# Optimization experiments

Hardware: AMD Instinct MI355X
Metric: run time of the kernel (lower is better)

The kernel has to match this reference:

```python
import jax, jax.numpy as jnp
import numpy as np

B, S, D, CH = 2048, 16, 512, 1024


def setup_inputs() -> dict:
    key = jax.random.key(0)
    ks = jax.random.split(key, 12)
    sc = lambda fan: 1.0 / np.sqrt(fan)
    return {
        "local_descs_t": jax.random.normal(ks[0], (B, S, D), jnp.float32),
        "local_descs_rot": jax.random.normal(ks[1], (B, S, D), jnp.float32),
        "w_scene": jax.random.normal(ks[2], (2 * D,), jnp.float32) * sc(2 * D),
        "b_scene": jnp.zeros((1,), jnp.float32),
        "Wh_t": jax.random.normal(ks[3], (S, D, CH), jnp.float32) * sc(D),
        "bh_t": jnp.zeros((S, CH), jnp.float32),
        "Wo_t": jax.random.normal(ks[4], (S, CH, 3), jnp.float32) * sc(CH),
        "bo_t": jnp.zeros((S, 3), jnp.float32),
        "Wh_r": jax.random.normal(ks[5], (S, D, CH), jnp.float32) * sc(D),
        "bh_r": jnp.zeros((S, CH), jnp.float32),
        "Wo_r": jax.random.normal(ks[6], (S, CH, 4), jnp.float32) * sc(CH),
        "bo_r": jnp.zeros((S, 4), jnp.float32),
    }


def _expert_head(x, onehot, Wh, bh, Wo, bo):
    # x: [B, D] gathered global descriptor; run all S experts, combine by one-hot
    h = jax.nn.gelu(jnp.einsum("bd,sdh->bsh", x, Wh) + bh, approximate=False)
    o = jnp.einsum("bsh,sho->bso", h, Wo) + bo  # [B, S, out]
    return jnp.einsum("bs,bso->bo", onehot, o)


def reference(local_descs_t, local_descs_rot, w_scene, b_scene,
              Wh_t, bh_t, Wo_t, bo_t, Wh_r, bh_r, Wo_r, bo_r):
    # scene router: Linear(2D -> 1) over concatenated descriptors, log_softmax over scenes
    cat = jnp.concatenate([local_descs_t, local_descs_rot], axis=2)  # [B, S, 2D]
    logits = jnp.einsum("bsd,d->bs", cat, w_scene) + b_scene[0]
    scene_log_distr = jax.nn.log_softmax(logits, axis=1)  # [B, S]
    max_indices = jnp.argmax(scene_log_distr, axis=1)  # [B]
    onehot = jax.nn.one_hot(max_indices, S, dtype=local_descs_t.dtype)
    # combine: gather selected scene's descriptor (torch code uses dense mask w)
    global_desc_t = jnp.einsum("bs,bsd->bd", onehot, local_descs_t)
    global_desc_rot = jnp.einsum("bs,bsd->bd", onehot, local_descs_rot)
    # per-sample expert heads (Linear -> GELU -> Linear)
    x_t = _expert_head(global_desc_t, onehot, Wh_t, bh_t, Wo_t, bo_t)    # [B, 3]
    x_rot = _expert_head(global_desc_rot, onehot, Wh_r, bh_r, Wo_r, bo_r)  # [B, 4]
    pose = jnp.concatenate([x_t, x_rot], axis=1)  # [B, 7]
    return pose, scene_log_distr
```

## Files before the change

### kernel.cpp

```cpp
#include <hip/hip_runtime.h>
#include <hip/hip_bf16.h>
#include <math.h>

constexpr int B_  = 2048;
constexpr int S_  = 16;
constexpr int D_  = 512;
constexpr int CH_ = 1024;

typedef __attribute__((ext_vector_type(8))) short bf16x8;
typedef __attribute__((ext_vector_type(4))) float f32x4;

constexpr size_t CNT_OFF  = 0;
constexpr size_t NT_OFF   = 64;
constexpr size_t TL_OFF   = 128;
constexpr size_t LIST_OFF = 512;
constexpr size_t XGT_OFF  = LIST_OFF + (size_t)16 * 2048 * 4;
constexpr size_t XGR_OFF  = XGT_OFF + (size_t)B_ * D_ * 2;

static __device__ __forceinline__ short f2bf(float x) {
    __hip_bfloat16 h = __float2bfloat16(x);
    return *(short*)&h;
}
static __device__ __forceinline__ float gelu_exact(float x) {
    return 0.5f * x * (1.f + erff(x * 0.70710678118654752f));
}

static __device__ __forceinline__ void gl_lds16(const void* g, void* l) {
    __builtin_amdgcn_global_load_lds(
        (const __attribute__((address_space(1))) void*)g,
        (__attribute__((address_space(3))) void*)l,
        16, 0, 0);
}

__global__ __launch_bounds__(1024) void k_router_sm(
    const float* __restrict__ ldt, const float* __restrict__ ldr,
    const float* __restrict__ w,   const float* __restrict__ bsc,
    float* __restrict__ sld, int* __restrict__ count, int* __restrict__ list,
    unsigned short* __restrict__ xgt, unsigned short* __restrict__ xgr,
    float* __restrict__ pose)
{
    const int b    = blockIdx.x;
    const int wave = threadIdx.x >> 6;
    const int lane = threadIdx.x & 63;

    __shared__ float lgs[S_];
    __shared__ int   smi;

    if (threadIdx.x < 7) pose[(size_t)b * 7 + threadIdx.x] = 0.f;

    const float4* pt = (const float4*)(ldt + ((size_t)b * S_ + wave) * D_);
    const float4* pr = (const float4*)(ldr + ((size_t)b * S_ + wave) * D_);
    const float4* wt = (const float4*)(w);
    const float4* wr = (const float4*)(w + D_);

    float acc = 0.f;
    #pragma unroll
    for (int it = 0; it < 2; it++) {
        const int i = lane + it * 64;
        float4 a  = pt[i]; float4 ww = wt[i];
        acc += a.x * ww.x + a.y * ww.y + a.z * ww.z + a.w * ww.w;
        float4 c  = pr[i]; float4 w2 = wr[i];
        acc += c.x * w2.x + c.y * w2.y + c.z * w2.z + c.w * w2.w;
    }
    #pragma unroll
    for (int off = 32; off > 0; off >>= 1) acc += __shfl_down(acc, off, 64);
    if (lane == 0) lgs[wave] = acc;
    __syncthreads();

    if (threadIdx.x < S_) {
        const int s = threadIdx.x;
        const float v = lgs[s] + bsc[0];
        float mv = v; int mi = s;
        #pragma unroll
        for (int d = 1; d < 16; d <<= 1) {
            float ov = __shfl_xor(mv, d, 16);
            int   oi = __shfl_xor(mi, d, 16);
            if (ov > mv || (ov == mv && oi < mi)) { mv = ov; mi = oi; }
        }
        float sum = expf(v - mv);
        #pragma unroll
        for (int d = 1; d < 16; d <<= 1) sum += __shfl_xor(sum, d, 16);
        const float lse = mv + logf(sum);
        sld[b * S_ + s] = v - lse;
        if (s == 0) {
            smi = mi;
            const int pos = atomicAdd(&count[mi], 1);
            list[mi * B_ + pos] = b;
        }
    }
    __syncthreads();

    const int mi = smi;
    const int t = threadIdx.x;
    if (t < D_) {
        xgt[(size_t)b * D_ + t] = (unsigned short)f2bf(ldt[((size_t)b * S_ + mi) * D_ + t]);
    } else {
        const int t2 = t - D_;
        xgr[(size_t)b * D_ + t2] = (unsigned short)f2bf(ldr[((size_t)b * S_ + mi) * D_ + t2]);
    }
}

__global__ void k_tiles(const int* __restrict__ count, int* __restrict__ ntile,
                        int* __restrict__ tlist)
{
    if (threadIdx.x == 0 && blockIdx.x == 0) {
        int nt = 0;
        for (int m = 0; m < S_; m++) {
            const int c = count[m];
            const int nst = (c + 63) >> 6;
            for (int s2 = 0; s2 < nst; s2++) tlist[nt++] = m | (s2 << 8);
        }
        ntile[0] = nt;
    }
}

__global__ __launch_bounds__(256) void k_expert(
    const float* __restrict__ Wht, const float* __restrict__ bht,
    const float* __restrict__ Wot, const float* __restrict__ bot,
    const float* __restrict__ Whr, const float* __restrict__ bhr,
    const float* __restrict__ Wor, const float* __restrict__ bor,
    const unsigned short* __restrict__ xgt, const unsigned short* __restrict__ xgr,
    const int* __restrict__ count, const int* __restrict__ list,
    const int* __restrict__ ntile, const int* __restrict__ tlist,
    float* __restrict__ pose)
{
    const int bid  = blockIdx.x;
    const int ct   = bid & 15;
    const int head = (bid >> 4) & 1;
    const int t    = bid >> 5;
    if (t >= ntile[0]) return;
    const int tv = tlist[t];
    const int m  = tv & 255;
    const int st = tv >> 8;
    const int n  = count[m];

    const unsigned short* __restrict__ xg = head ? xgr : xgt;
    const float* __restrict__ Wh = head ? Whr : Wht;
    const float* __restrict__ bh = head ? bhr : bht;
    const float* __restrict__ Wo = head ? Wor : Wot;
    const float* __restrict__ bo = head ? bor : bot;
    const int noj    = head ? 4 : 3;
    const int jobase = head ? 3 : 0;
    const int ch0    = ct * 64;

    __shared__ short As[64 * 64];
    __shared__ float Bsf[64 * 64];
    __shared__ float ored[64][4];
    __shared__ int   bidx[64];

    const int tid  = threadIdx.x;
    const int wave = tid >> 6;
    const int lane = tid & 63;
    const int l15  = lane & 15;
    const int lq   = lane >> 4;
    const int wr   = wave >> 1, wc = wave & 1;
    const int rbase = wr * 32, cbase = wc * 32;

    if (tid < 64) {
        const int gi = st * 64 + tid;
        bidx[tid] = (gi < n) ? list[m * B_ + gi] : list[m * B_];
    }
    ((float*)ored)[tid] = 0.f;
    __syncthreads();

    const unsigned short* gA[2];
    #pragma unroll
    for (int i = 0; i < 2; i++) {
        const int r = (wave * 2 + i) * 8 + (lane >> 3);
        const int c = (lane & 7) ^ (r & 7);
        gA[i] = xg + (size_t)bidx[r] * D_ + c * 8;
    }
    const float* gB[4];
    #pragma unroll
    for (int i = 0; i < 4; i++) {
        const int q2 = wave * 4 + i;
        gB[i] = Wh + (size_t)m * D_ * CH_ + (size_t)(q2 * 4 + (lane >> 4)) * CH_ + ch0 + (l15 * 4);
    }

    f32x4 acc[2][2] = {};

    for (int kt = 0; kt < 8; kt++) {
        const int k0 = kt * 64;
        #pragma unroll
        for (int i = 0; i < 2; i++)
            gl_lds16(gA[i] + k0, &As[(wave * 2 + i) * 512]);
        #pragma unroll
        for (int i = 0; i < 4; i++)
            gl_lds16(gB[i] + (size_t)k0 * CH_, &Bsf[(wave * 4 + i) * 256]);
        __syncthreads();

        #pragma unroll
        for (int ks = 0; ks < 2; ks++) {
            bf16x8 a[2];
            #pragma unroll
            for (int fm = 0; fm < 2; fm++) {
                const int r = rbase + fm * 16 + l15;
                const int u = ks * 4 + lq;
                a[fm] = *(const bf16x8*)&As[r * 64 + ((u ^ (r & 7)) << 3)];
            }
            bf16x8 bv[2];
            #pragma unroll
            for (int fn = 0; fn < 2; fn++) {
                const int c = cbase + fn * 16 + l15;
                const int kb = ks * 32 + lq * 8;
                short tmp[8];
                #pragma unroll
                for (int j = 0; j < 8; j++) tmp[j] = f2bf(Bsf[(kb + j) * 64 + c]);
                bv[fn] = *(bf16x8*)tmp;
            }
            #pragma unroll
            for (int fm = 0; fm < 2; fm++)
                #pragma unroll
                for (int fn = 0; fn < 2; fn++)
                    acc[fm][fn] = __builtin_amdgcn_mfma_f32_16x16x32_bf16(a[fm], bv[fn], acc[fm][fn], 0, 0, 0);
        }
        __syncthreads();
    }

    float g[2][2][4];
    float wo_l[2][4];
    #pragma unroll
    for (int fn = 0; fn < 2; fn++) {
        const int ch = ch0 + cbase + fn * 16 + l15;
        const float bias = bh[m * CH_ + ch];
        #pragma unroll
        for (int fm = 0; fm < 2; fm++)
            #pragma unroll
            for (int j = 0; j < 4; j++)
                g[fm][fn][j] = gelu_exact(acc[fm][fn][j] + bias);
        #pragma unroll
        for (int jo = 0; jo < 4; jo++)
            wo_l[fn][jo] = (jo < noj) ? Wo[(size_t)(m * CH_ + ch) * noj + jo] : 0.f;
    }

    #pragma unroll
    for (int fm = 0; fm < 2; fm++) {
        #pragma unroll
        for (int j = 0; j < 4; j++) {
            const int rl = rbase + fm * 16 + lq * 4 + j;
            #pragma unroll
            for (int jo = 0; jo < 4; jo++) {
                if (jo >= noj) continue;
                float v = g[fm][0][j] * wo_l[0][jo] + g[fm][1][j] * wo_l[1][jo];
                #pragma unroll
                for (int d = 1; d < 16; d <<= 1) v += __shfl_xor(v, d, 16);
                if (l15 == 0)
                    atomicAdd(&ored[rl][jo], v);
            }
        }
    }
    __syncthreads();

    {
        const int rl = tid >> 2;
        const int jo = tid & 3;
        const int gi = st * 64 + rl;
        if (jo < noj && gi < n) {
            const int bb = list[m * B_ + gi];
            float v = ored[rl][jo];
            if (ct == 0) v += bo[m * noj + jo];
            atomicAdd(&pose[(size_t)bb * 7 + jobase + jo], v);
        }
    }
}

extern "C" void kernel_launch(void* const* d_in, const int* in_sizes, int n_in,
                              void* d_out, int out_size, void* d_ws, size_t ws_size,
                              hipStream_t stream)
{
    const float* ldt = (const float*)d_in[0];
    const float* ldr = (const float*)d_in[1];
    const float* wsc = (const float*)d_in[2];
    const float* bsc = (const float*)d_in[3];
    const float* Wht = (const float*)d_in[4];
    const float* bht = (const float*)d_in[5];
    const float* Wot = (const float*)d_in[6];
    const float* bot = (const float*)d_in[7];
    const float* Whr = (const float*)d_in[8];
    const float* bhr = (const float*)d_in[9];
    const float* Wor = (const float*)d_in[10];
    const float* bor = (const float*)d_in[11];

    float* pose = (float*)d_out;
    float* sld  = (float*)d_out + (size_t)B_ * 7;

    int* count = (int*)((char*)d_ws + CNT_OFF);
    int* ntile = (int*)((char*)d_ws + NT_OFF);
    int* tlist = (int*)((char*)d_ws + TL_OFF);
    int* list  = (int*)((char*)d_ws + LIST_OFF);
    unsigned short* xgt = (unsigned short*)((char*)d_ws + XGT_OFF);
    unsigned short* xgr = (unsigned short*)((char*)d_ws + XGR_OFF);

    (void)hipMemsetAsync(count, 0, 16 * sizeof(int), stream);

    k_router_sm<<<dim3(B_), dim3(1024), 0, stream>>>(
        ldt, ldr, wsc, bsc, sld, count, list, xgt, xgr, pose);

    k_tiles<<<dim3(1), dim3(64), 0, stream>>>(count, ntile, tlist);

    k_expert<<<dim3(48 * 2 * 16), dim3(256), 0, stream>>>(
        Wht, bht, Wot, bot, Whr, bhr, Wor, bor,
        xgt, xgr, count, list, ntile, tlist, pose);
}
```

Before: 78.12 us.

## Fuse tile-list build into router via last-block counter and shrink router blocks

The separate single-thread k_tiles kernel is removed. The router kernel's last-finishing block, found through a global done counter with a threadfence and atomic, now builds the tile list, which saves one kernel launch and its dependency gap. The router block size drops from 1024 to 256 threads, so each wave reduces four scenes, and the descriptor gather and bf16 conversion now use float4 loads with short4 stores. The memset is widened to also clear the done counter. This relies on correct atomic visibility of count across blocks.

Result: slower. 133.3 us (+70.6%).

```diff
diff --git a/kernel.cpp b/kernel.cpp
--- a/kernel.cpp
+++ b/kernel.cpp
@@ -11,7 +11,8 @@
 typedef __attribute__((ext_vector_type(4))) float f32x4;
 
 constexpr size_t CNT_OFF  = 0;
-constexpr size_t NT_OFF   = 64;
+constexpr size_t DONE_OFF = 64;
+constexpr size_t NT_OFF   = 96;
 constexpr size_t TL_OFF   = 128;
 constexpr size_t LIST_OFF = 512;
 constexpr size_t XGT_OFF  = LIST_OFF + (size_t)16 * 2048 * 4;
@@ -32,43 +33,55 @@
         16, 0, 0);
 }
 
-__global__ __launch_bounds__(1024) void k_router_sm(
+__global__ __launch_bounds__(256) void k_router_sm(
     const float* __restrict__ ldt, const float* __restrict__ ldr,
     const float* __restrict__ w,   const float* __restrict__ bsc,
     float* __restrict__ sld, int* __restrict__ count, int* __restrict__ list,
     unsigned short* __restrict__ xgt, unsigned short* __restrict__ xgr,
-    float* __restrict__ pose)
+    float* __restrict__ pose, int* __restrict__ done,
+    int* __restrict__ ntile, int* __restrict__ tlist)
 {
     const int b    = blockIdx.x;
-    const int wave = threadIdx.x >> 6;
-    const int lane = threadIdx.x & 63;
+    const int tid  = threadIdx.x;
+    const int wave = tid >> 6;
+    const int lane = tid & 63;
 
     __shared__ float lgs[S_];
     __shared__ int   smi;
 
-    if (threadIdx.x < 7) pose[(size_t)b * 7 + threadIdx.x] = 0.f;
-
-    const float4* pt = (const float4*)(ldt + ((size_t)b * S_ + wave) * D_);
-    const float4* pr = (const float4*)(ldr + ((size_t)b * S_ + wave) * D_);
+    if (tid < 7) pose[(size_t)b * 7 + tid] = 0.f;
+
     const float4* wt = (const float4*)(w);
     const float4* wr = (const float4*)(w + D_);
 
-    float acc = 0.f;
-    #pragma unroll
-    for (int it = 0; it < 2; it++) {
-        const int i = lane + it * 64;
-        float4 a  = pt[i]; float4 ww = wt[i];
-        acc += a.x * ww.x + a.y * ww.y + a.z * ww.z + a.w * ww.w;
-        float4 c  = pr[i]; float4 w2 = wr[i];
-        acc += c.x * w2.x + c.y * w2.y + c.z * w2.z + c.w * w2.w;
-    }
-    #pragma unroll
-    for (int off = 32; off > 0; off >>= 1) acc += __shfl_down(acc, off, 64);
-    if (lane == 0) lgs[wave] = acc;
-    __syncthreads();
-
-    if (threadIdx.x < S_) {
-        const int s = threadIdx.x;
+    float accv[4];
+    #pragma unroll
+    for (int it = 0; it < 4; it++) {
+        const int s = wave * 4 + it;
+        const float4* pt = (const float4*)(ldt + ((size_t)b * S_ + s) * D_);
+        const float4* pr = (const float4*)(ldr + ((size_t)b * S_ + s) * D_);
+        float a = 0.f;
+        #pragma unroll
+        for (int half = 0; half < 2; half++) {
+            const int i = lane + half * 64;
+            const float4 x  = pt[i]; const float4 ww = wt[i];
+            a += x.x * ww.x + x.y * ww.y + x.z * ww.z + x.w * ww.w;
+            const float4 y  = pr[i]; const float4 w2 = wr[i];
+            a += y.x * w2.x + y.y * w2.y + y.z * w2.z + y.w * w2.w;
+        }
+        accv[it] = a;
+    }
+    #pragma unroll
+    for (int it = 0; it < 4; it++) {
+        float a = accv[it];
+        #pragma unroll
+        for (int off = 32; off > 0; off >>= 1) a += __shfl_down(a, off, 64);
+        if (lane == 0) lgs[wave * 4 + it] = a;
+    }
+    __syncthreads();
+
+    if (tid < S_) {
+        const int s = tid;
         const float v = lgs[s] + bsc[0];
         float mv = v; int mi = s;
         #pragma unroll
@@ -91,26 +104,29 @@
     __syncthreads();
 
     const int mi = smi;
-    const int t = threadIdx.x;
-    if (t < D_) {
-        xgt[(size_t)b * D_ + t] = (unsigned short)f2bf(ldt[((size_t)b * S_ + mi) * D_ + t]);
+    if (tid < 128) {
+        const float4 v = ((const float4*)(ldt + ((size_t)b * S_ + mi) * D_))[tid];
+        short4 o; o.x = f2bf(v.x); o.y = f2bf(v.y); o.z = f2bf(v.z); o.w = f2bf(v.w);
+        *reinterpret_cast<short4*>(&xgt[(size_t)b * D_ + (size_t)tid * 4]) = o;
     } else {
-        const int t2 = t - D_;
-        xgr[(size_t)b * D_ + t2] = (unsigned short)f2bf(ldr[((size_t)b * S_ + mi) * D_ + t2]);
-    }
-}
-
-__global__ void k_tiles(const int* __restrict__ count, int* __restrict__ ntile,
-                        int* __restrict__ tlist)
-{
-    if (threadIdx.x == 0 && blockIdx.x == 0) {
-        int nt = 0;
-        for (int m = 0; m < S_; m++) {
-            const int c = count[m];
-            const int nst = (c + 63) >> 6;
-            for (int s2 = 0; s2 < nst; s2++) tlist[nt++] = m | (s2 << 8);
-        }
-        ntile[0] = nt;
+        const int t2 = tid - 128;
+        const float4 v = ((const float4*)(ldr + ((size_t)b * S_ + mi) * D_))[t2];
+        short4 o; o.x = f2bf(v.x); o.y = f2bf(v.y); o.z = f2bf(v.z); o.w = f2bf(v.w);
+        *reinterpret_cast<short4*>(&xgr[(size_t)b * D_ + (size_t)t2 * 4]) = o;
+    }
+    __syncthreads();
+
+    if (tid == 0) {
+        __threadfence();
+        if (atomicAdd(done, 1) == (int)gridDim.x - 1) {
+            int nt = 0;
+            for (int mm = 0; mm < S_; mm++) {
+                const int c = atomicAdd(&count[mm], 0);
+                const int nst = (c + 63) >> 6;
+                for (int s2 = 0; s2 < nst; s2++) tlist[nt++] = mm | (s2 << 8);
+            }
+            ntile[0] = nt;
+        }
     }
 }
 
@@ -285,18 +301,17 @@
     float* sld  = (float*)d_out + (size_t)B_ * 7;
 
     int* count = (int*)((char*)d_ws + CNT_OFF);
+    int* done  = (int*)((char*)d_ws + DONE_OFF);
     int* ntile = (int*)((char*)d_ws + NT_OFF);
     int* tlist = (int*)((char*)d_ws + TL_OFF);
     int* list  = (int*)((char*)d_ws + LIST_OFF);
     unsigned short* xgt = (unsigned short*)((char*)d_ws + XGT_OFF);
     unsigned short* xgr = (unsigned short*)((char*)d_ws + XGR_OFF);
 
-    (void)hipMemsetAsync(count, 0, 16 * sizeof(int), stream);
-
-    k_router_sm<<<dim3(B_), dim3(1024), 0, stream>>>(
-        ldt, ldr, wsc, bsc, sld, count, list, xgt, xgr, pose);
-
-    k_tiles<<<dim3(1), dim3(64), 0, stream>>>(count, ntile, tlist);
+    (void)hipMemsetAsync(d_ws, 0, 128, stream);
+
+    k_router_sm<<<dim3(B_), dim3(256), 0, stream>>>(
+        ldt, ldr, wsc, bsc, sld, count, list, xgt, xgr, pose, done, ntile, tlist);
 
     k_expert<<<dim3(48 * 2 * 16), dim3(256), 0, stream>>>(
         Wht, bht, Wot, bot, Whr, bhr, Wor, bor,
```

## Split router into batched logits kernel and per-sample finish kernel

Applied to the files above, without the earlier changes.

The fused 1024-thread router kernel is replaced by two kernels. k_logits has each wave handle four (batch, scene) rows, with the scene weights hoisted into registers and all row loads issued before any reduction, to raise memory-level parallelism on the large descriptor stream. k_finish uses one wave per sample to do log-softmax, argmax, list append and a vectorized bf16 gather of the selected rows. The cost is an extra kernel launch, a small logits round trip through workspace, and a second read of the selected descriptor rows.

Measured after the change: 90.73 us. 1.16x slower.

```diff
diff --git a/kernel.cpp b/kernel.cpp
--- a/kernel.cpp
+++ b/kernel.cpp
@@ -11,9 +11,10 @@
 typedef __attribute__((ext_vector_type(4))) float f32x4;
 
 constexpr size_t CNT_OFF  = 0;
-constexpr size_t NT_OFF   = 64;
+constexpr size_t NT_OFF   = 96;
 constexpr size_t TL_OFF   = 128;
-constexpr size_t LIST_OFF = 512;
+constexpr size_t LOG_OFF  = 384;
+constexpr size_t LIST_OFF = LOG_OFF + (size_t)B_ * S_ * 4;
 constexpr size_t XGT_OFF  = LIST_OFF + (size_t)16 * 2048 * 4;
 constexpr size_t XGR_OFF  = XGT_OFF + (size_t)B_ * D_ * 2;
 
@@ -23,6 +24,9 @@
 }
 static __device__ __forceinline__ float gelu_exact(float x) {
     return 0.5f * x * (1.f + erff(x * 0.70710678118654752f));
+}
+static __device__ __forceinline__ float dot4(float4 a, float4 b) {
+    return a.x * b.x + a.y * b.y + a.z * b.z + a.w * b.w;
 }
 
 static __device__ __forceinline__ void gl_lds16(const void* g, void* l) {
@@ -32,71 +36,83 @@
         16, 0, 0);
 }
 
-__global__ __launch_bounds__(1024) void k_router_sm(
+__global__ __launch_bounds__(256, 4) void k_logits(
     const float* __restrict__ ldt, const float* __restrict__ ldr,
     const float* __restrict__ w,   const float* __restrict__ bsc,
+    float* __restrict__ logits)
+{
+    const int lane = threadIdx.x & 63;
+    const int wid  = blockIdx.x * 4 + (threadIdx.x >> 6);
+    const int p0   = wid * 4;
+
+    const float4* wt = (const float4*)w;
+    const float4 wv0 = wt[lane];
+    const float4 wv1 = wt[lane + 64];
+    const float4 wv2 = wt[lane + 128];
+    const float4 wv3 = wt[lane + 192];
+    const float bias = bsc[0];
+
+    float4 xt[4][2], xr[4][2];
+    #pragma unroll
+    for (int k = 0; k < 4; k++) {
+        const float4* pt = (const float4*)(ldt + (size_t)(p0 + k) * D_);
+        const float4* pr = (const float4*)(ldr + (size_t)(p0 + k) * D_);
+        xt[k][0] = pt[lane]; xt[k][1] = pt[lane + 64];
+        xr[k][0] = pr[lane]; xr[k][1] = pr[lane + 64];
+    }
+    #pragma unroll
+    for (int k = 0; k < 4; k++) {
+        float a = dot4(xt[k][0], wv0) + dot4(xt[k][1], wv1)
+                + dot4(xr[k][0], wv2) + dot4(xr[k][1], wv3);
+        #pragma unroll
+        for (int off = 32; off > 0; off >>= 1) a += __shfl_down(a, off, 64);
+        if (lane == 0) logits[p0 + k] = a + bias;
+    }
+}
+
+__global__ __launch_bounds__(256) void k_finish(
+    const float* __restrict__ ldt, const float* __restrict__ ldr,
+    const float* __restrict__ logits,
     float* __restrict__ sld, int* __restrict__ count, int* __restrict__ list,
     unsigned short* __restrict__ xgt, unsigned short* __restrict__ xgr,
     float* __restrict__ pose)
 {
-    const int b    = blockIdx.x;
     const int wave = threadIdx.x >> 6;
     const int lane = threadIdx.x & 63;
-
-    __shared__ float lgs[S_];
-    __shared__ int   smi;
-
-    if (threadIdx.x < 7) pose[(size_t)b * 7 + threadIdx.x] = 0.f;
-
-    const float4* pt = (const float4*)(ldt + ((size_t)b * S_ + wave) * D_);
-    const float4* pr = (const float4*)(ldr + ((size_t)b * S_ + wave) * D_);
-    const float4* wt = (const float4*)(w);
-    const float4* wr = (const float4*)(w + D_);
-
-    float acc = 0.f;
-    #pragma unroll
-    for (int it = 0; it < 2; it++) {
-        const int i = lane + it * 64;
-        float4 a  = pt[i]; float4 ww = wt[i];
-        acc += a.x * ww.x + a.y * ww.y + a.z * ww.z + a.w * ww.w;
-        float4 c  = pr[i]; float4 w2 = wr[i];
-        acc += c.x * w2.x + c.y * w2.y + c.z * w2.z + c.w * w2.w;
-    }
-    #pragma unroll
-    for (int off = 32; off > 0; off >>= 1) acc += __shfl_down(acc, off, 64);
-    if (lane == 0) lgs[wave] = acc;
-    __syncthreads();
-
-    if (threadIdx.x < S_) {
-        const int s = threadIdx.x;
-        const float v = lgs[s] + bsc[0];
-        float mv = v; int mi = s;
-        #pragma unroll
-        for (int d = 1; d < 16; d <<= 1) {
-            float ov = __shfl_xor(mv, d, 16);
-            int   oi = __shfl_xor(mi, d, 16);
-            if (ov > mv || (ov == mv && oi < mi)) { mv = ov; mi = oi; }
-        }
-        float sum = expf(v - mv);
-        #pragma unroll
-        for (int d = 1; d < 16; d <<= 1) sum += __shfl_xor(sum, d, 16);
-        const float lse = mv + logf(sum);
-        sld[b * S_ + s] = v - lse;
-        if (s == 0) {
-            smi = mi;
-            const int pos = atomicAdd(&count[mi], 1);
-            list[mi * B_ + pos] = b;
-        }
-    }
-    __syncthreads();
-
-    const int mi = smi;
-    const int t = threadIdx.x;
-    if (t < D_) {
-        xgt[(size_t)b * D_ + t] = (unsigned short)f2bf(ldt[((size_t)b * S_ + mi) * D_ + t]);
-    } else {
-        const int t2 = t - D_;
-        xgr[(size_t)b * D_ + t2] = (unsigned short)f2bf(ldr[((size_t)b * S_ + mi) * D_ + t2]);
+    const int b    = blockIdx.x * 4 + wave;
+
+    float v = (lane < S_) ? logits[b * S_ + lane] : -INFINITY;
+    float mv = v; int mi_ = lane;
+    #pragma unroll
+    for (int d = 1; d < 16; d <<= 1) {
+        float ov = __shfl_xor(mv, d, 16);
+        int   oi = __shfl_xor(mi_, d, 16);
+        if (ov > mv || (ov == mv && oi < mi_)) { mv = ov; mi_ = oi; }
+    }
+    float e = (lane < S_) ? expf(v - mv) : 0.f;
+    float sum = e;
+    #pragma unroll
+    for (int d = 1; d < 16; d <<= 1) sum += __shfl_xor(sum, d, 16);
+    if (lane < S_) sld[b * S_ + lane] = v - (mv + logf(sum));
+
+    const int mi = __shfl(mi_, 0, 64);
+    if (lane == 0) {
+        const int pos = atomicAdd(&count[mi], 1);
+        list[mi * B_ + pos] = b;
+    }
+    if (lane < 7) pose[(size_t)b * 7 + lane] = 0.f;
+
+    const float4* pt = (const float4*)(ldt + ((size_t)b * S_ + mi) * D_);
+    const float4* pr = (const float4*)(ldr + ((size_t)b * S_ + mi) * D_);
+    #pragma unroll
+    for (int h = 0; h < 2; h++) {
+        const int i = lane + h * 64;
+        const float4 a = pt[i];
+        short4 o1; o1.x = f2bf(a.x); o1.y = f2bf(a.y); o1.z = f2bf(a.z); o1.w = f2bf(a.w);
+        *reinterpret_cast<short4*>(&xgt[(size_t)b * D_ + (size_t)i * 4]) = o1;
+        const float4 c = pr[i];
+        short4 o2; o2.x = f2bf(c.x); o2.y = f2bf(c.y); o2.z = f2bf(c.z); o2.w = f2bf(c.w);
+        *reinterpret_cast<short4*>(&xgr[(size_t)b * D_ + (size_t)i * 4]) = o2;
     }
 }
 
@@ -284,17 +300,20 @@
     float* pose = (float*)d_out;
     float* sld  = (float*)d_out + (size_t)B_ * 7;
 
-    int* count = (int*)((char*)d_ws + CNT_OFF);
-    int* ntile = (int*)((char*)d_ws + NT_OFF);
-    int* tlist = (int*)((char*)d_ws + TL_OFF);
-    int* list  = (int*)((char*)d_ws + LIST_OFF);
+    int*   count  = (int*)((char*)d_ws + CNT_OFF);
+    int*   ntile  = (int*)((char*)d_ws + NT_OFF);
+    int*   tlist  = (int*)((char*)d_ws + TL_OFF);
+    float* logits = (float*)((char*)d_ws + LOG_OFF);
+    int*   list   = (int*)((char*)d_ws + LIST_OFF);
     unsigned short* xgt = (unsigned short*)((char*)d_ws + XGT_OFF);
     unsigned short* xgr = (unsigned short*)((char*)d_ws + XGR_OFF);
 
-    (void)hipMemsetAsync(count, 0, 16 * sizeof(int), stream);
-
-    k_router_sm<<<dim3(B_), dim3(1024), 0, stream>>>(
-        ldt, ldr, wsc, bsc, sld, count, list, xgt, xgr, pose);
+    (void)hipMemsetAsync(count, 0, 64, stream);
+
+    k_logits<<<dim3(B_ * S_ / 16), dim3(256), 0, stream>>>(ldt, ldr, wsc, bsc, logits);
+
+    k_finish<<<dim3(B_ / 4), dim3(256), 0, stream>>>(
+        ldt, ldr, logits, sld, count, list, xgt, xgr, pose);
 
     k_tiles<<<dim3(1), dim3(64), 0, stream>>>(count, ntile, tlist);
 
```
